# Kernel tuning notes

Hardware: AMD Instinct MI355X
Metric: run time of the kernel (lower is better)

The kernel has to match this reference:

```python
import jax, jax.numpy as jnp
import numpy as np


def _quant_dequant_rowwise(v):
    # vector-wise absmax int8 quantization along the last axis, then dequant.
    # Exactly reproduces dequantized result of the int8 GEMM operand:
    # Cx = round(v/s) clipped to [-127,127]; dq = Cx * s.
    s = jnp.max(jnp.abs(v), axis=-1, keepdims=True) / 127.0
    s = jnp.maximum(s, 1e-8)
    q = jnp.clip(jnp.round(v / s), -127.0, 127.0)
    return q * s


def setup_inputs() -> dict:
    key = jax.random.key(0)
    k1, k2, k3 = jax.random.split(key, 3)
    B, S, K, N = 4, 2048, 4096, 4096
    x = jax.random.normal(k1, (B, S, K), dtype=jnp.float32)
    # amplify a few feature columns so |col| exceeds the 6.0 outlier threshold,
    # exercising the LLM.int8() mixed-precision decomposition path
    x = x.at[..., ::256].multiply(10.0)
    W = jax.random.normal(k2, (N, K), dtype=jnp.float32) * 0.02
    bias = jax.random.normal(k3, (N,), dtype=jnp.float32) * 0.01
    return {"x": x, "W": W, "bias": bias, "threshold": 6}


def reference(x, W, bias, threshold):
    # LLM.int8() matmul with outlier decomposition (bnb.matmul semantics):
    #  1. columns of x whose absmax > threshold are outliers -> fp16/fp32 path
    #  2. remaining x columns + full W are vector-wise int8 quantized, int8 GEMM,
    #     dequant with per-row scales (exactly equal to dq(x) @ dq(W).T)
    #  3. out = int8-part + x_outlier @ W_outlier.T + bias
    thr = jnp.asarray(threshold, dtype=x.dtype)
    B_shape = x.shape[:-1]
    K = x.shape[-1]
    x2 = x.reshape(-1, K)                                   # [M, K]
    colmax = jnp.max(jnp.abs(x2), axis=0)                   # [K]
    out_mask = (colmax > thr).astype(x.dtype)               # 1.0 on outlier cols
    x_int = x2 * (1.0 - out_mask)                           # zero outlier cols
    dq_x = _quant_dequant_rowwise(x_int)                    # [M, K]
    dq_w = _quant_dequant_rowwise(W)                        # [N, K]
    out = dq_x @ dq_w.T                                     # int8 GEMM, dequantized
    out = out + (x2 * out_mask) @ (W * out_mask).T          # fp outlier GEMM
    out = out + bias
    return out.reshape(*B_shape, W.shape[0])
```

## Files before the change

### kernel.cpp

```cpp
#include <hip/hip_runtime.h>

typedef unsigned short u16;
typedef unsigned char u8;
typedef unsigned int u32;
typedef __attribute__((ext_vector_type(4))) float f32x4;
typedef __attribute__((ext_vector_type(16))) float f32x16;
typedef __attribute__((ext_vector_type(8))) __bf16 bf16x8;
typedef __attribute__((ext_vector_type(4))) int i32x4;
typedef __attribute__((ext_vector_type(16))) int i32x16;

__device__ __forceinline__ u16 f2bf(float f) {
  u32 u = __float_as_uint(f);
  u32 r = (u + 0x7fffu + ((u >> 16) & 1u)) >> 16;
  return (u16)r;
}

__device__ __forceinline__ float load_thr(const int* p) {
  int iv = *p;
  float fv = __int_as_float(iv);
  if (fv >= 1.0f && fv <= 1.0e6f) return fv;
  return (float)iv;
}

__device__ __forceinline__ void gload_lds16(const void* g, void* l) {
  __builtin_amdgcn_global_load_lds(
      (const __attribute__((address_space(1))) void*)g,
      (__attribute__((address_space(3))) void*)l, 16, 0, 0);
}

__global__ void k_init_cm(u32* cm, int K) {
  int i = blockIdx.x * 256 + threadIdx.x;
  if (i < K) cm[i] = 0u;
}

__global__ __launch_bounds__(256) void k_colmax(const float* __restrict__ x,
                                                u32* __restrict__ cm, int M,
                                                int K, int rpb) {
  int c4 = blockIdx.x * 256 + threadIdx.x;
  int r0 = blockIdx.y * rpb;
  int r1 = r0 + rpb;
  if (r1 > M) r1 = M;
  f32x4 mx = {0.f, 0.f, 0.f, 0.f};
  for (int r = r0; r < r1; ++r) {
    f32x4 v = *(const f32x4*)&x[(size_t)r * K + (size_t)c4 * 4];
#pragma unroll
    for (int i = 0; i < 4; ++i) mx[i] = fmaxf(mx[i], fabsf(v[i]));
  }
#pragma unroll
  for (int i = 0; i < 4; ++i)
    atomicMax(&cm[c4 * 4 + i], __float_as_uint(mx[i]));
}

__global__ void k_ocols(const u32* __restrict__ cm, const int* __restrict__ thr_i,
                        int K, int* __restrict__ meta) {
  int lane = threadIdx.x;
  float thr = load_thr(thr_i);
  const float* cmf = (const float*)cm;
  int per = K >> 6;
  int base = lane * per;
  int c = 0;
  for (int i = 0; i < per; ++i) c += (cmf[base + i] > thr) ? 1 : 0;
  int inc = c;
  for (int off = 1; off < 64; off <<= 1) {
    int t = __shfl_up(inc, off);
    if (lane >= off) inc += t;
  }
  int excl = inc - c;
  int total = __shfl(inc, 63);
  if (lane == 0) meta[0] = total < 64 ? total : 64;
  int idx = excl;
  for (int i = 0; i < per; ++i) {
    if (cmf[base + i] > thr) {
      if (idx < 64) meta[1 + idx] = base + i;
      idx++;
    }
  }
  for (int j = total + lane; j < 64; j += 64) meta[1 + j] = -1;
}

__global__ __launch_bounds__(256) void k_quant8(
    const float* __restrict__ src, const u32* __restrict__ cm,
    const int* __restrict__ thr_i, const int* __restrict__ meta,
    char* __restrict__ qdst, float* __restrict__ sdst, u16* __restrict__ odst,
    int K, int zero_outlier) {
  int row = blockIdx.x;
  int tid = threadIdx.x;
  float thr = load_thr(thr_i);
  const float* sr = src + (size_t)row * K;
  const float* cmf = (const float*)cm;

  float v[16];
  u32 omask = 0;
  float lmax = 0.f;
#pragma unroll
  for (int j = 0; j < 4; ++j) {
    int c4 = j * 256 + tid;
    f32x4 val = *(const f32x4*)&sr[c4 * 4];
    f32x4 cv = *(const f32x4*)&cmf[c4 * 4];
#pragma unroll
    for (int i = 0; i < 4; ++i) {
      float xv = val[i];
      v[j * 4 + i] = xv;
      bool is_out = cv[i] > thr;
      if (is_out) omask |= 1u << (j * 4 + i);
      if (!is_out || !zero_outlier) lmax = fmaxf(lmax, fabsf(xv));
    }
  }
  float m = lmax;
#pragma unroll
  for (int off = 32; off >= 1; off >>= 1) m = fmaxf(m, __shfl_down(m, off));
  __shared__ float red[4];
  int lane = tid & 63, wv = tid >> 6;
  if (lane == 0) red[wv] = m;
  __syncthreads();
  float rm = fmaxf(fmaxf(red[0], red[1]), fmaxf(red[2], red[3]));
  float s = fmaxf(rm / 127.0f, 1e-8f);

  u32* qt = (u32*)qdst;
  size_t rowpart = (size_t)(row >> 5) * (K >> 5) * 256 + (size_t)(row & 31) * 8;
#pragma unroll
  for (int j = 0; j < 4; ++j) {
    int c4 = j * 256 + tid;
    u32 pk = 0;
#pragma unroll
    for (int i = 0; i < 4; ++i) {
      float xv = v[j * 4 + i];
      int iq;
      if (zero_outlier && (omask & (1u << (j * 4 + i)))) {
        iq = 0;
      } else {
        float q = rintf(xv / s);
        q = fminf(fmaxf(q, -127.f), 127.f);
        iq = (int)q;
      }
      pk |= ((u32)(u8)(char)iq) << (8 * i);
    }
    qt[rowpart + (size_t)(c4 >> 3) * 256 + (c4 & 7)] = pk;
  }
  if (tid == 0) sdst[row] = s;
  if (tid < 64) {
    int n_out = meta[0];
    int oc = meta[1 + tid];
    u16 ov = 0;
    if (tid < n_out && oc >= 0) ov = f2bf(sr[oc]);
    odst[(size_t)row * 64 + tid] = ov;
  }
}

__global__ __launch_bounds__(512, 4) void k_gemm_i8(
    const char* __restrict__ qx, const char* __restrict__ qw,
    const float* __restrict__ sx, const float* __restrict__ sw,
    const float* __restrict__ bias, const char* __restrict__ xo,
    const char* __restrict__ wo, float* __restrict__ out, int M, int N,
    int K) {
  extern __shared__ char lds_raw[];
  int tid = threadIdx.x;
  int lane = tid & 63, wave = tid >> 6;
  int wm = wave >> 2, wn = wave & 3;

  int nwg = gridDim.x, bid = blockIdx.x;
  int swzb = (bid & 7) * (nwg >> 3) + (bid >> 3);
  int nbn = N >> 8;
  int bm = swzb / nbn, bn = swzb % nbn;
  int r0 = bm << 7, c0 = bn << 8;
  int K32 = K >> 5;

  const char* asrc;
  {
    int b = tid >> 6, mb = b >> 1, kb = b & 1, u = tid & 63;
    asrc = qx + ((size_t)((r0 >> 5) + mb) * K32 + kb) * 1024 + (u & 31) * 32 +
           (u >> 5) * 16;
  }
  const char* bsrc0;
  const char* bsrc1;
  {
    int g = tid, b = g >> 6, nb = b >> 1, kb = b & 1, u = g & 63;
    bsrc0 = qw + ((size_t)((c0 >> 5) + nb) * K32 + kb) * 1024 + (u & 31) * 32 +
            (u >> 5) * 16;
    g = tid + 512; b = g >> 6; nb = b >> 1; kb = b & 1; u = g & 63;
    bsrc1 = qw + ((size_t)((c0 >> 5) + nb) * K32 + kb) * 1024 + (u & 31) * 32 +
            (u >> 5) * 16;
  }

#define BUF0 (lds_raw)
#define BUF1 (lds_raw + 24576)
#define STAGE(bufp, kt)                                                       \
  {                                                                           \
    gload_lds16(asrc + (((kt) >> 5) << 10), (bufp) + tid * 16);               \
    gload_lds16(bsrc0 + (((kt) >> 5) << 10), (bufp) + 8192 + tid * 16);       \
    gload_lds16(bsrc1 + (((kt) >> 5) << 10),                                  \
                (bufp) + 8192 + (tid + 512) * 16);                            \
  }

#define LDAI(dst, bufp, q, ks)                                                \
  dst = *(const i32x4*)((bufp) + (((wm * 2 + (q)) * 2 + (ks)) << 10) +        \
                        lane * 16);
#define LDBI(dst, bufp, nf, ks)                                               \
  dst = *(const i32x4*)((bufp) + 8192 +                                       \
                        (((wn * 2 + (nf)) * 2 + (ks)) << 10) + lane * 16);

#define MFI(q, nf, av, bv)                                                    \
  acc[q][nf] =                                                                \
      __builtin_amdgcn_mfma_i32_32x32x32_i8(av, bv, acc[q][nf], 0, 0, 0)

#define TILE(bufc, bufn, kt, ktn)                                             \
  {                                                                           \
    STAGE(bufn, ktn);                                                         \
    asm volatile("s_waitcnt vmcnt(3)" ::: "memory");                          \
    __builtin_amdgcn_s_barrier();                                             \
    i32x4 a00, a01, a10, a11, b00, b01, b10, b11;                             \
    LDAI(a00, bufc, 0, 0);                                                    \
    LDAI(a01, bufc, 0, 1);                                                    \
    LDAI(a10, bufc, 1, 0);                                                    \
    LDAI(a11, bufc, 1, 1);                                                    \
    LDBI(b00, bufc, 0, 0);                                                    \
    LDBI(b01, bufc, 0, 1);                                                    \
    LDBI(b10, bufc, 1, 0);                                                    \
    LDBI(b11, bufc, 1, 1);                                                    \
    asm volatile("s_waitcnt lgkmcnt(0)" ::: "memory");                        \
    __builtin_amdgcn_s_setprio(1);                                            \
    MFI(0, 0, a00, b00);                                                      \
    MFI(0, 1, a00, b10);                                                      \
    MFI(1, 0, a10, b00);                                                      \
    MFI(1, 1, a10, b10);                                                      \
    MFI(0, 0, a01, b01);                                                      \
    MFI(0, 1, a01, b11);                                                      \
    MFI(1, 0, a11, b01);                                                      \
    MFI(1, 1, a11, b11);                                                      \
    __builtin_amdgcn_s_setprio(0);                                            \
    __builtin_amdgcn_s_barrier();                                             \
  }

  i32x16 acc[2][2] = {};

  STAGE(BUF0, 0);

  int NT = K >> 6;
  for (int t = 0; t < NT; t += 2) {
    int kt1 = (t + 1) << 6;
    int kt2 = (t + 2) < NT ? (t + 2) << 6 : 0;
    TILE(BUF0, BUF1, t << 6, kt1);
    TILE(BUF1, BUF0, kt1, kt2);
  }

  asm volatile("s_waitcnt vmcnt(0)" ::: "memory");
  __builtin_amdgcn_s_barrier();

#pragma unroll
  for (int i = 0; i < 2; ++i) {
    int g = tid + i * 512;
    int rw = g >> 3;
    int cb = ((g & 7) ^ (rw & 7)) << 4;
    gload_lds16(xo + (size_t)(r0 + rw) * 128 + cb, lds_raw + g * 16);
  }
#pragma unroll
  for (int i = 0; i < 4; ++i) {
    int g = tid + i * 512;
    int rw = g >> 3;
    int cb = ((g & 7) ^ (rw & 7)) << 4;
    gload_lds16(wo + (size_t)(c0 + rw) * 128 + cb, lds_raw + 16384 + g * 16);
  }

  f32x16 facc[2][2];
  float swv[2], bv[2];
#pragma unroll
  for (int nf = 0; nf < 2; ++nf) {
    swv[nf] = sw[c0 + wn * 64 + nf * 32 + (lane & 31)];
    bv[nf] = bias[c0 + wn * 64 + nf * 32 + (lane & 31)];
  }
#pragma unroll
  for (int q = 0; q < 2; ++q) {
    int gmb = r0 + wm * 64 + q * 32 + 4 * (lane >> 5);
    f32x4 s4a = *(const f32x4*)&sx[gmb];
    f32x4 s4b = *(const f32x4*)&sx[gmb + 8];
    f32x4 s4c = *(const f32x4*)&sx[gmb + 16];
    f32x4 s4d = *(const f32x4*)&sx[gmb + 24];
#pragma unroll
    for (int reg = 0; reg < 16; ++reg) {
      float sxv = (reg < 4) ? s4a[reg & 3]
                : (reg < 8) ? s4b[reg & 3]
                : (reg < 12) ? s4c[reg & 3] : s4d[reg & 3];
#pragma unroll
      for (int nf = 0; nf < 2; ++nf)
        facc[q][nf][reg] = (float)acc[q][nf][reg] * sxv * swv[nf];
    }
  }

  asm volatile("s_waitcnt vmcnt(0)" ::: "memory");
  __builtin_amdgcn_s_barrier();

#pragma unroll
  for (int ks = 0; ks < 4; ++ks) {
    bf16x8 ob[2];
#pragma unroll
    for (int nf = 0; nf < 2; ++nf) {
      int rn = wn * 64 + nf * 32 + (lane & 31);
      ob[nf] = *(const bf16x8*)(lds_raw + 16384 + rn * 128 +
                                (((ks * 2 + (lane >> 5)) ^ (rn & 7)) << 4));
    }
#pragma unroll
    for (int q = 0; q < 2; ++q) {
      int rl = wm * 64 + q * 32 + (lane & 31);
      bf16x8 oa = *(const bf16x8*)(lds_raw + rl * 128 +
                                   (((ks * 2 + (lane >> 5)) ^ (rl & 7)) << 4));
#pragma unroll
      for (int nf = 0; nf < 2; ++nf)
        facc[q][nf] = __builtin_amdgcn_mfma_f32_32x32x16_bf16(
            oa, ob[nf], facc[q][nf], 0, 0, 0);
    }
  }

#pragma unroll
  for (int q = 0; q < 2; ++q) {
#pragma unroll
    for (int reg = 0; reg < 16; ++reg) {
      int gm = r0 + wm * 64 + q * 32 + (reg & 3) + 8 * (reg >> 2) +
               4 * (lane >> 5);
      float* orow = out + (size_t)gm * N + c0 + wn * 64 + (lane & 31);
#pragma unroll
      for (int nf = 0; nf < 2; ++nf)
        orow[nf * 32] = facc[q][nf][reg] + bv[nf];
    }
  }
}

extern "C" void kernel_launch(void* const* d_in, const int* in_sizes, int n_in,
                              void* d_out, int out_size, void* d_ws,
                              size_t ws_size, hipStream_t stream) {
  const float* x = (const float*)d_in[0];
  const float* W = (const float*)d_in[1];
  const float* bias = (const float*)d_in[2];
  const int* thr = (const int*)d_in[3];
  float* out = (float*)d_out;

  int N = in_sizes[2];
  int K = in_sizes[1] / N;
  int M = in_sizes[0] / K;

  char* ws = (char*)d_ws;
  u32* cm = (u32*)ws;
  int* meta = (int*)(ws + 16384);
  float* sx = (float*)(ws + 32768);
  float* sw = (float*)(ws + 32768 + (size_t)M * 4);
  char* xo = ws + 32768 + (size_t)(M + N) * 4;
  char* wo = xo + (size_t)M * 128;
  char* qx = wo + (size_t)N * 128;
  char* qw = qx + (size_t)M * K;

  k_init_cm<<<dim3((K + 255) / 256), dim3(256), 0, stream>>>(cm, K);

  {
    int gx = K / 1024;
    int gy = 128;
    int rpb = (M + gy - 1) / gy;
    k_colmax<<<dim3(gx, gy), dim3(256), 0, stream>>>(x, cm, M, K, rpb);
  }

  k_ocols<<<dim3(1), dim3(64), 0, stream>>>(cm, thr, K, meta);

  k_quant8<<<dim3(M), dim3(256), 0, stream>>>(x, cm, thr, meta, qx, sx,
                                              (u16*)xo, K, 1);
  k_quant8<<<dim3(N), dim3(256), 0, stream>>>(W, cm, thr, meta, qw, sw,
                                              (u16*)wo, K, 0);

  (void)hipFuncSetAttribute((const void*)k_gemm_i8,
                            hipFuncAttributeMaxDynamicSharedMemorySize,
                            49152);
  int nwg = (M / 128) * (N / 256);
  k_gemm_i8<<<dim3(nwg), dim3(512), 49152, stream>>>(qx, qw, sx, sw, bias,
                                                     xo, wo, out, M, N, K);
}
```

Baseline: 263.7 us.

## Load W int8 fragments directly from global into registers, bypassing LDS

The W operand tiles are no longer staged through shared memory. Each wave loads its B fragments straight from global memory into registers in MFMA-ready layout, and only the A tile is double-buffered in LDS, which shrinks the LDS footprint. This removes the LDS write/read traffic for B and may raise occupancy. In exchange, the B global loads are no longer prefetched a tile ahead, so their latency sits on the critical path. Waves sharing the same wn also reload the same W data redundantly, relying on the cache to absorb it.

```diff
diff --git a/kernel.cpp b/kernel.cpp
--- a/kernel.cpp
+++ b/kernel.cpp
@@ -164,6 +164,7 @@
   int bm = swzb / nbn, bn = swzb % nbn;
   int r0 = bm << 7, c0 = bn << 8;
   int K32 = K >> 5;
+  int bperm = (lane & 31) * 32 + (lane >> 5) * 16;
 
   const char* asrc;
   {
@@ -171,33 +172,20 @@
     asrc = qx + ((size_t)((r0 >> 5) + mb) * K32 + kb) * 1024 + (u & 31) * 32 +
            (u >> 5) * 16;
   }
-  const char* bsrc0;
-  const char* bsrc1;
-  {
-    int g = tid, b = g >> 6, nb = b >> 1, kb = b & 1, u = g & 63;
-    bsrc0 = qw + ((size_t)((c0 >> 5) + nb) * K32 + kb) * 1024 + (u & 31) * 32 +
-            (u >> 5) * 16;
-    g = tid + 512; b = g >> 6; nb = b >> 1; kb = b & 1; u = g & 63;
-    bsrc1 = qw + ((size_t)((c0 >> 5) + nb) * K32 + kb) * 1024 + (u & 31) * 32 +
-            (u >> 5) * 16;
-  }
+  const char* bbase0 =
+      qw + ((size_t)((c0 >> 5) + wn * 2) * K32 << 10) + bperm;
+  const char* bbase1 = bbase0 + ((size_t)K32 << 10);
 
 #define BUF0 (lds_raw)
-#define BUF1 (lds_raw + 24576)
-#define STAGE(bufp, kt)                                                       \
-  {                                                                           \
-    gload_lds16(asrc + (((kt) >> 5) << 10), (bufp) + tid * 16);               \
-    gload_lds16(bsrc0 + (((kt) >> 5) << 10), (bufp) + 8192 + tid * 16);       \
-    gload_lds16(bsrc1 + (((kt) >> 5) << 10),                                  \
-                (bufp) + 8192 + (tid + 512) * 16);                            \
-  }
+#define BUF1 (lds_raw + 8192)
+#define STAGE_A(bufp, kt) \
+  gload_lds16(asrc + (((kt) >> 5) << 10), (bufp) + tid * 16);
 
 #define LDAI(dst, bufp, q, ks)                                                \
   dst = *(const i32x4*)((bufp) + (((wm * 2 + (q)) * 2 + (ks)) << 10) +        \
                         lane * 16);
-#define LDBI(dst, bufp, nf, ks)                                               \
-  dst = *(const i32x4*)((bufp) + 8192 +                                       \
-                        (((wn * 2 + (nf)) * 2 + (ks)) << 10) + lane * 16);
+#define LDBG(dst, base, kt, ks)                                               \
+  dst = *(const i32x4*)((base) + ((size_t)(((kt) >> 5) + (ks)) << 10));
 
 #define MFI(q, nf, av, bv)                                                    \
   acc[q][nf] =                                                                \
@@ -205,18 +193,19 @@
 
 #define TILE(bufc, bufn, kt, ktn)                                             \
   {                                                                           \
-    STAGE(bufn, ktn);                                                         \
-    asm volatile("s_waitcnt vmcnt(3)" ::: "memory");                          \
+    i32x4 b00, b01, b10, b11;                                                 \
+    LDBG(b00, bbase0, kt, 0);                                                 \
+    LDBG(b01, bbase0, kt, 1);                                                 \
+    LDBG(b10, bbase1, kt, 0);                                                 \
+    LDBG(b11, bbase1, kt, 1);                                                 \
+    STAGE_A(bufn, ktn);                                                       \
+    asm volatile("s_waitcnt vmcnt(1)" ::: "memory");                          \
     __builtin_amdgcn_s_barrier();                                             \
-    i32x4 a00, a01, a10, a11, b00, b01, b10, b11;                             \
+    i32x4 a00, a01, a10, a11;                                                 \
     LDAI(a00, bufc, 0, 0);                                                    \
     LDAI(a01, bufc, 0, 1);                                                    \
     LDAI(a10, bufc, 1, 0);                                                    \
     LDAI(a11, bufc, 1, 1);                                                    \
-    LDBI(b00, bufc, 0, 0);                                                    \
-    LDBI(b01, bufc, 0, 1);                                                    \
-    LDBI(b10, bufc, 1, 0);                                                    \
-    LDBI(b11, bufc, 1, 1);                                                    \
     asm volatile("s_waitcnt lgkmcnt(0)" ::: "memory");                        \
     __builtin_amdgcn_s_setprio(1);                                            \
     MFI(0, 0, a00, b00);                                                      \
@@ -233,7 +222,7 @@
 
   i32x16 acc[2][2] = {};
 
-  STAGE(BUF0, 0);
+  STAGE_A(BUF0, 0);
 
   int NT = K >> 6;
   for (int t = 0; t < NT; t += 2) {
```

New measurement: 281.4 us. +6.7%, slower.
